# Kernel tuning notes

Measured on AMD Instinct MI355X. Metric: run time of the kernel, lower is better.

The kernel has to match this reference:

```python
import jax, jax.numpy as jnp
import numpy as np

N = 4096
IN_C = 256
F = 256          # num_filter
C = 40           # label_dim
KP1 = 3          # K+1 Chebyshev orders (K=2 hardcoded in forward)
E = 131072
TWO_PI = 2.0 * np.pi


def build_Lc(edges, q, edge_weight, n):
    """Conjugate of the normalized magnetic Laplacian (max_eigen=2 => L = -A_n * exp(i*Theta)).
    We return conj(L) because the original code swaps L.real/L.imag when feeding `process`,
    which is algebraically O_i = i * conj(T_i(L))."""
    row, col = edges[0], edges[1]
    A = jnp.zeros((n, n), jnp.float32).at[row, col].add(edge_weight)  # duplicates sum, as in coo_matrix
    A_sym = 0.5 * (A + A.T)
    d = A_sym.sum(axis=0)
    d = jnp.where(d == 0, 1.0, d)
    dinv = d ** -0.5
    A_n = dinv[:, None] * A_sym * dinv[None, :]
    Theta = TWO_PI * q * (A - A.T)
    # conj(L) = -A_n * exp(-i*Theta)
    return (-A_n).astype(jnp.complex64) * jnp.exp(-1j * Theta.astype(jnp.complex64))


def cheb_layer(Lc, Xr, Xi, W, b):
    """One ChebConv_Qin_Direct layer. Output = sum_i (i * T_i(conj(L)) @ Xc) @ W_i + bias,
    which reproduces the real/imag-swapped `process` of the original module."""
    Xc = (Xr + 1j * Xi).astype(jnp.complex64)      # [N, d]
    Z0 = Xc
    Z1 = Lc @ Xc                                   # sparse-equivalent spmm, dense here
    Z2 = 2.0 * (Lc @ Z1) - Z0                      # Chebyshev recursion T2 = 2 L T1 - T0
    Yc = 1j * (Z0 @ W[0].astype(jnp.complex64)
               + Z1 @ W[1].astype(jnp.complex64)
               + Z2 @ W[2].astype(jnp.complex64))  # [N, out]
    return Yc.real + b, Yc.imag + b


def setup_inputs() -> dict:
    key = jax.random.key(0)
    k = jax.random.split(key, 8)
    stdv1 = 1.0 / np.sqrt(F)
    return {
        "real": jax.random.normal(k[0], (N, IN_C), jnp.float32),
        "imag": jax.random.normal(k[1], (N, IN_C), jnp.float32),
        "edges": jax.random.randint(k[2], (2, E), 0, N),
        "q": jnp.float32(0.25),
        "edge_weight": jax.random.uniform(k[3], (E,), jnp.float32),
        "W1": jax.random.uniform(k[4], (KP1, IN_C, F), jnp.float32, -stdv1, stdv1),
        "b1": jnp.zeros((1, F), jnp.float32),
        "W2": jax.random.uniform(k[5], (KP1, F, F), jnp.float32, -stdv1, stdv1),
        "b2": jnp.zeros((1, F), jnp.float32),
        "Wc": jax.random.normal(k[6], (C, 2 * F), jnp.float32) * (1.0 / np.sqrt(2 * F)),
        "bc": jnp.zeros((C,), jnp.float32),
    }


def reference(real, imag, edges, q, edge_weight, W1, b1, W2, b2, Wc, bc):
    n = real.shape[0]
    Lc = build_Lc(edges, q, edge_weight, n)        # same L is rebuilt each layer in the original
    r, i = cheb_layer(Lc, real, imag, W1, b1)
    r, i = cheb_layer(Lc, r, i, W2, b2)            # activation=False, dropout=False
    x = jnp.concatenate([r, i], axis=-1)           # [N, 2F]
    logits = x @ Wc.T + bc                         # Conv1d(kernel_size=1) == linear
    return jax.nn.log_softmax(logits, axis=-1)     # [N, C]
```

## Files before the change

kernel.cpp:

```cpp
#include <hip/hip_runtime.h>
#include <cmath>

#define N_NODES 4096
#define FDIM    256
#define CDIM    40
#define NEDGE   131072
#define CAP     256
#define HBITS   20
#define HSIZE   (1 << HBITS)
#define TWO_PI_F 6.28318530717958647692f

typedef __bf16 bf16;
typedef __bf16 bf16x2 __attribute__((ext_vector_type(2)));
typedef __bf16 bf16x4 __attribute__((ext_vector_type(4)));
typedef __bf16 bf16x8 __attribute__((ext_vector_type(8)));
typedef float  f32x4  __attribute__((ext_vector_type(4)));

static constexpr size_t NF = (size_t)N_NODES * FDIM;

struct __align__(16) Entry { float lr, li; int col, pad; };

__device__ __forceinline__ void gld_lds16(const bf16* g, bf16* s) {
    __builtin_amdgcn_global_load_lds(
        (const __attribute__((address_space(1))) void*)g,
        (__attribute__((address_space(3))) void*)s,
        16, 0, 0);
}

__device__ __forceinline__ unsigned cell_hash(unsigned cell) {
    return (cell * 2654435761u) >> (32 - HBITS);
}

__global__ void hash_insert(const int* __restrict__ edges,
                            const float* __restrict__ ew,
                            int* __restrict__ hkey, float* __restrict__ hval,
                            float* __restrict__ rowsum, float* __restrict__ colsum) {
    int e = blockIdx.x * blockDim.x + threadIdx.x;
    if (e >= NEDGE) return;
    int r = edges[e], c = edges[NEDGE + e];
    float wv = ew[e];
    atomicAdd(rowsum + r, wv);
    atomicAdd(colsum + c, wv);
    unsigned cell = (unsigned)r * N_NODES + c;
    unsigned h = cell_hash(cell);
    for (;;) {
        int old = atomicCAS(hkey + h, 0, (int)(cell + 1));
        if (old == 0 || old == (int)(cell + 1)) { atomicAdd(hval + h, wv); break; }
        h = (h + 1) & (HSIZE - 1);
    }
}

__global__ __launch_bounds__(256) void hash_to_ell(
    const int* __restrict__ hkey, const float* __restrict__ hval,
    const float* __restrict__ rowsum, const float* __restrict__ colsum,
    const float* __restrict__ qptr,
    int* __restrict__ cnt, Entry* __restrict__ ent) {
    int h = blockIdx.x * 256 + threadIdx.x;
    int k = hkey[h];
    if (k == 0) return;
    unsigned cell = (unsigned)(k - 1);
    int i = cell >> 12, j = cell & 4095;
    float a = hval[h];
    float b = 0.f;
    bool mirror = false;
    if (i == j) { b = a; mirror = true; }
    else {
        unsigned mcell = (unsigned)j * N_NODES + i;
        unsigned hh = cell_hash(mcell);
        for (;;) {
            int kk = hkey[hh];
            if (kk == (int)(mcell + 1)) { b = hval[hh]; mirror = true; break; }
            if (kk == 0) break;
            hh = (hh + 1) & (HSIZE - 1);
        }
    }
    float di = 0.5f * (rowsum[i] + colsum[i]); if (di == 0.f) di = 1.f;
    float dj = 0.5f * (rowsum[j] + colsum[j]); if (dj == 0.f) dj = 1.f;
    float an = 0.5f * (a + b) / sqrtf(di * dj);
    float s, c;
    sincosf(TWO_PI_F * qptr[0] * (a - b), &s, &c);
    int pos = atomicAdd(cnt + i, 1);
    if (pos < CAP) {
        Entry en; en.lr = -an * c; en.li = an * s; en.col = j; en.pad = 0;
        ent[(size_t)i * CAP + pos] = en;
    }
    if (!mirror) {
        int pos2 = atomicAdd(cnt + j, 1);
        if (pos2 < CAP) {
            Entry en; en.lr = -an * c; en.li = -an * s; en.col = i; en.pad = 0;
            ent[(size_t)j * CAP + pos2] = en;
        }
    }
}

__global__ __launch_bounds__(256) void cast_in2(const float* __restrict__ Xr,
                                                const float* __restrict__ Xi,
                                                bf16* __restrict__ Xr16,
                                                bf16* __restrict__ Xi16,
                                                bf16* __restrict__ XC) {
    int idx = blockIdx.x * 256 + threadIdx.x;
    float vr = Xr[idx], vi = Xi[idx];
    Xr16[idx] = (bf16)vr; Xi16[idx] = (bf16)vi;
    bf16x2 p; p[0] = (bf16)vr; p[1] = (bf16)vi;
    ((bf16x2*)XC)[idx] = p;
}

#define NWT (256 * 768)
__global__ __launch_bounds__(256) void cast_weights(
    const float* __restrict__ W1, const float* __restrict__ W2,
    const float* __restrict__ Wc,
    bf16* __restrict__ W1t, bf16* __restrict__ W2t, bf16* __restrict__ Wcb) {
    int idx = blockIdx.x * 256 + threadIdx.x;
    if (idx < 2 * NWT) {
        const float* W = (idx < NWT) ? W1 : W2;
        bf16* Wt = (idx < NWT) ? W1t : W2t;
        int id = (idx < NWT) ? idx : idx - NWT;
        int nout = id / 768, kk = id - nout * 768;
        int o = kk >> 8, k = kk & 255;
        Wt[id] = (bf16)W[((size_t)o * 256 + k) * 256 + nout];
    } else {
        int id = idx - 2 * NWT;
        if (id < 48 * 512) {
            int row = id >> 9, k = id & 511;
            Wcb[id] = (row < CDIM) ? (bf16)Wc[row * 512 + k] : (bf16)0.f;
        }
    }
}

__global__ __launch_bounds__(256) void spmm_k(
    const int* __restrict__ cnt, const Entry* __restrict__ ent,
    const bf16* __restrict__ XC,
    const bf16* __restrict__ C0C,
    float alpha, float beta,
    bf16* __restrict__ Zr, bf16* __restrict__ Zi, bf16* __restrict__ ZC)
{
    __shared__ f32x4 redR[3][64];
    __shared__ f32x4 redI[3][64];

    const int wave = threadIdx.x >> 6, lane = threadIdx.x & 63;
    const int row = blockIdx.x;
    int n1 = cnt[row]; if (n1 > CAP) n1 = CAP;
    const Entry* erow = ent + (size_t)row * CAP;

    float ar[4] = {}, ai[4] = {};
    int e = wave;
    for (; e + 12 < n1; e += 16) {
        Entry e0 = erow[e];
        Entry e1 = erow[e + 4];
        Entry e2 = erow[e + 8];
        Entry e3 = erow[e + 12];
        bf16x8 x0 = *(const bf16x8*)&XC[(size_t)(e0.col & 4095) * 512 + lane * 8];
        bf16x8 x1 = *(const bf16x8*)&XC[(size_t)(e1.col & 4095) * 512 + lane * 8];
        bf16x8 x2 = *(const bf16x8*)&XC[(size_t)(e2.col & 4095) * 512 + lane * 8];
        bf16x8 x3 = *(const bf16x8*)&XC[(size_t)(e3.col & 4095) * 512 + lane * 8];
        #pragma unroll
        for (int c = 0; c < 4; ++c) {
            float xr, xi;
            xr = (float)x0[2 * c]; xi = (float)x0[2 * c + 1];
            ar[c] += e0.lr * xr - e0.li * xi;  ai[c] += e0.lr * xi + e0.li * xr;
            xr = (float)x1[2 * c]; xi = (float)x1[2 * c + 1];
            ar[c] += e1.lr * xr - e1.li * xi;  ai[c] += e1.lr * xi + e1.li * xr;
            xr = (float)x2[2 * c]; xi = (float)x2[2 * c + 1];
            ar[c] += e2.lr * xr - e2.li * xi;  ai[c] += e2.lr * xi + e2.li * xr;
            xr = (float)x3[2 * c]; xi = (float)x3[2 * c + 1];
            ar[c] += e3.lr * xr - e3.li * xi;  ai[c] += e3.lr * xi + e3.li * xr;
        }
    }
    for (; e < n1; e += 4) {
        Entry e0 = erow[e];
        bf16x8 x0 = *(const bf16x8*)&XC[(size_t)(e0.col & 4095) * 512 + lane * 8];
        #pragma unroll
        for (int c = 0; c < 4; ++c) {
            float xr0 = (float)x0[2 * c], xi0 = (float)x0[2 * c + 1];
            ar[c] += e0.lr * xr0 - e0.li * xi0;
            ai[c] += e0.lr * xi0 + e0.li * xr0;
        }
    }

    if (wave != 0) {
        f32x4 r, i;
        #pragma unroll
        for (int c = 0; c < 4; ++c) { r[c] = ar[c]; i[c] = ai[c]; }
        redR[wave - 1][lane] = r;
        redI[wave - 1][lane] = i;
    }
    __syncthreads();
    if (wave != 0) return;

    #pragma unroll
    for (int w = 0; w < 3; ++w) {
        f32x4 r = redR[w][lane], i = redI[w][lane];
        #pragma unroll
        for (int c = 0; c < 4; ++c) { ar[c] += r[c]; ai[c] += i[c]; }
    }

    float vr[4], vi[4];
    if (beta != 0.f) {
        bf16x8 c0 = *(const bf16x8*)&C0C[(size_t)row * 512 + lane * 8];
        #pragma unroll
        for (int c = 0; c < 4; ++c) {
            vr[c] = alpha * ar[c] + beta * (float)c0[2 * c];
            vi[c] = alpha * ai[c] + beta * (float)c0[2 * c + 1];
        }
    } else {
        #pragma unroll
        for (int c = 0; c < 4; ++c) { vr[c] = alpha * ar[c]; vi[c] = alpha * ai[c]; }
    }
    size_t base = (size_t)row * FDIM + lane * 4;
    bf16x4 pr, pi;
    #pragma unroll
    for (int c = 0; c < 4; ++c) { pr[c] = (bf16)vr[c]; pi[c] = (bf16)vi[c]; }
    *(bf16x4*)&Zr[base] = pr;
    *(bf16x4*)&Zi[base] = pi;
    if (ZC) {
        bf16x8 o;
        #pragma unroll
        for (int c = 0; c < 4; ++c) { o[2 * c] = pr[c]; o[2 * c + 1] = pi[c]; }
        *(bf16x8*)&ZC[(size_t)row * 512 + lane * 8] = o;
    }
}

__global__ __launch_bounds__(256) void wapply_mfma(
    const bf16* __restrict__ Z0r, const bf16* __restrict__ Z0i,
    const bf16* __restrict__ Z1r, const bf16* __restrict__ Z1i,
    const bf16* __restrict__ Z2r, const bf16* __restrict__ Z2i,
    const bf16* __restrict__ Wt,
    const float* __restrict__ bias,
    float* __restrict__ O32r, float* __restrict__ O32i,
    bf16* __restrict__ O16r_r, bf16* __restrict__ O16r_i,
    bf16* __restrict__ OC)
{
    __shared__ __align__(16) bf16 sZr[64 * 32];
    __shared__ __align__(16) bf16 sZi[64 * 32];
    __shared__ __align__(16) bf16 sW [64 * 32];

    const int tid  = threadIdx.x;
    const int wave = tid >> 6;
    const int lane = tid & 63;
    const int rowBase = blockIdx.y * 64;
    const int colBase = blockIdx.x * 64;

    const int srow = lane >> 2;
    const int skc  = (lane & 3) * 8;

    f32x4 accSr[2][2] = {}, accSi[2][2] = {};
    const int wm = wave & 1, wn = wave >> 1;
    const int fr = lane & 15;
    const int fk = (lane >> 4) * 8;

    for (int kb = 0; kb < 3 * FDIM; kb += 32) {
        int order = kb >> 8;
        int kloc  = kb & 255;
        if (wave == 0 || wave == 1) {
            const bf16* z;
            if (wave == 0) z = (order == 0) ? Z0r : (order == 1) ? Z1r : Z2r;
            else           z = (order == 0) ? Z0i : (order == 1) ? Z1i : Z2i;
            bf16* s = (wave == 0) ? sZr : sZi;
            const bf16* g = z + (size_t)(rowBase + srow) * FDIM + kloc + skc;
            #pragma unroll
            for (int t = 0; t < 4; ++t)
                gld_lds16(g + (size_t)t * 16 * FDIM, s + t * 512);
        } else if (wave == 2) {
            const bf16* g = Wt + (size_t)(colBase + srow) * 768 + kb + skc;
            #pragma unroll
            for (int t = 0; t < 4; ++t)
                gld_lds16(g + (size_t)t * 16 * 768, sW + t * 512);
        }
        __syncthreads();

        bf16x8 zr[2], zi[2], wv[2];
        #pragma unroll
        for (int m = 0; m < 2; ++m) {
            int r = wm * 32 + m * 16 + fr;
            zr[m] = *(const bf16x8*)&sZr[r * 32 + fk];
            zi[m] = *(const bf16x8*)&sZi[r * 32 + fk];
        }
        #pragma unroll
        for (int n = 0; n < 2; ++n) {
            int c = wn * 32 + n * 16 + fr;
            wv[n] = *(const bf16x8*)&sW[c * 32 + fk];
        }
        #pragma unroll
        for (int m = 0; m < 2; ++m)
            #pragma unroll
            for (int n = 0; n < 2; ++n) {
                accSr[m][n] = __builtin_amdgcn_mfma_f32_16x16x32_bf16(zr[m], wv[n], accSr[m][n], 0, 0, 0);
                accSi[m][n] = __builtin_amdgcn_mfma_f32_16x16x32_bf16(zi[m], wv[n], accSi[m][n], 0, 0, 0);
            }
        __syncthreads();
    }

    #pragma unroll
    for (int m = 0; m < 2; ++m)
        #pragma unroll
        for (int n = 0; n < 2; ++n) {
            int row0 = rowBase + wm * 32 + m * 16 + (lane >> 4) * 4;
            int col  = colBase + wn * 32 + n * 16 + (lane & 15);
            float bv = bias[col];
            #pragma unroll
            for (int r = 0; r < 4; ++r) {
                float vr = bv - accSi[m][n][r];
                float vi = bv + accSr[m][n][r];
                int row = row0 + r;
                size_t idx = (size_t)row * FDIM + col;
                if (O32r) {
                    O32r[idx] = vr; O32i[idx] = vi;
                }
                if (O16r_r) {
                    O16r_r[idx] = (bf16)vr; O16r_i[idx] = (bf16)vi;
                }
                if (OC) {
                    bf16x2 p; p[0] = (bf16)vr; p[1] = (bf16)vi;
                    ((bf16x2*)OC)[idx] = p;
                }
            }
        }
}

__global__ __launch_bounds__(256) void head_mfma(
    const bf16* __restrict__ Yrb,
    const bf16* __restrict__ Yib,
    const bf16* __restrict__ Wcb,
    const float* __restrict__ bc,
    float* __restrict__ out)
{
    __shared__ __align__(16) bf16 sY[64][72];
    __shared__ __align__(16) bf16 sW[48][72];
    __shared__ float sS[64][52];

    const int tid  = threadIdx.x;
    const int wave = tid >> 6;
    const int lane = tid & 63;
    const int r0 = blockIdx.x * 64;

    f32x4 acc[3] = {};

    for (int kb = 0; kb < 512; kb += 64) {
        const bf16* src = (kb < 256) ? Yrb : Yib;
        const int koff = kb & 255;
        #pragma unroll
        for (int e = 0; e < 2; ++e) {
            int idx = tid + e * 256;
            int rr = idx >> 3, kk = (idx & 7) * 8;
            *(bf16x8*)&sY[rr][kk] =
                *(const bf16x8*)&src[(size_t)(r0 + rr) * FDIM + koff + kk];
        }
        #pragma unroll
        for (int e = 0; e < 2; ++e) {
            int idx = tid + e * 256;
            if (idx < 384) {
                int rr = idx >> 3, kk = (idx & 7) * 8;
                *(bf16x8*)&sW[rr][kk] =
                    *(const bf16x8*)&Wcb[(size_t)rr * 512 + kb + kk];
            }
        }
        __syncthreads();
        #pragma unroll
        for (int ks = 0; ks < 2; ++ks) {
            bf16x8 a = *(const bf16x8*)&sY[wave * 16 + (lane & 15)][ks * 32 + (lane >> 4) * 8];
            #pragma unroll
            for (int n = 0; n < 3; ++n) {
                bf16x8 b = *(const bf16x8*)&sW[n * 16 + (lane & 15)][ks * 32 + (lane >> 4) * 8];
                acc[n] = __builtin_amdgcn_mfma_f32_16x16x32_bf16(a, b, acc[n], 0, 0, 0);
            }
        }
        __syncthreads();
    }

    #pragma unroll
    for (int n = 0; n < 3; ++n) {
        int col = n * 16 + (lane & 15);
        int rloc = wave * 16 + (lane >> 4) * 4;
        #pragma unroll
        for (int r = 0; r < 4; ++r)
            sS[rloc + r][col] = acc[n][r];
    }
    __syncthreads();

    if (tid < 64) {
        float mx = -INFINITY;
        #pragma unroll 8
        for (int c = 0; c < CDIM; ++c) {
            float lv = sS[tid][c] + bc[c];
            sS[tid][c] = lv;
            mx = fmaxf(mx, lv);
        }
        float se = 0.f;
        #pragma unroll 8
        for (int c = 0; c < CDIM; ++c) se += expf(sS[tid][c] - mx);
        float lse = mx + logf(se);
        #pragma unroll 8
        for (int c = 0; c < CDIM; ++c)
            out[(size_t)(r0 + tid) * CDIM + c] = sS[tid][c] - lse;
    }
}

extern "C" void kernel_launch(void* const* d_in, const int* in_sizes, int n_in,
                              void* d_out, int out_size, void* d_ws, size_t ws_size,
                              hipStream_t stream) {
    const float* real = (const float*)d_in[0];
    const float* imag = (const float*)d_in[1];
    const int*   edges = (const int*)d_in[2];
    const float* q    = (const float*)d_in[3];
    const float* ew   = (const float*)d_in[4];
    const float* W1   = (const float*)d_in[5];
    const float* b1   = (const float*)d_in[6];
    const float* W2   = (const float*)d_in[7];
    const float* b2   = (const float*)d_in[8];
    const float* Wc   = (const float*)d_in[9];
    const float* bc   = (const float*)d_in[10];
    float* out = (float*)d_out;

    char* w = (char*)d_ws;
    int*      hkey   = (int*)w;   w += (size_t)HSIZE * 4;
    float*    hval   = (float*)w; w += (size_t)HSIZE * 4;
    int*      cnt    = (int*)w;   w += N_NODES * 4;
    float*    rowsum = (float*)w; w += N_NODES * 4;
    float*    colsum = (float*)w; w += N_NODES * 4;
    size_t zero_bytes = (size_t)((char*)w - (char*)d_ws);
    Entry* ent  = (Entry*)w; w += (size_t)N_NODES * CAP * 16;
    bf16* Xr16 = (bf16*)w; w += NF * 2;
    bf16* Xi16 = (bf16*)w; w += NF * 2;
    bf16* XC   = (bf16*)w; w += NF * 4;
    bf16* Z1r  = (bf16*)w; w += NF * 2;
    bf16* Z1i  = (bf16*)w; w += NF * 2;
    bf16* Z1C  = (bf16*)w; w += NF * 4;
    bf16* Z2r  = (bf16*)w; w += NF * 2;
    bf16* Z2i  = (bf16*)w; w += NF * 2;
    float* Y1r32 = (float*)w; w += NF * 4;
    float* Y1i32 = (float*)w; w += NF * 4;
    bf16* Y1rb = (bf16*)w; w += NF * 2;
    bf16* Y1ib = (bf16*)w; w += NF * 2;
    bf16* Y1C  = (bf16*)w; w += NF * 4;
    bf16* Y2rb = (bf16*)w; w += NF * 2;
    bf16* Y2ib = (bf16*)w; w += NF * 2;
    bf16* W1t  = (bf16*)w; w += 256 * 768 * 2;
    bf16* W2t  = (bf16*)w; w += 256 * 768 * 2;
    bf16* Wcb  = (bf16*)w; w += 48 * 512 * 2;

    hipMemsetAsync(d_ws, 0, zero_bytes, stream);

    hash_insert<<<(NEDGE + 255) / 256, 256, 0, stream>>>(edges, ew, hkey, hval,
                                                         rowsum, colsum);
    hash_to_ell<<<HSIZE / 256, 256, 0, stream>>>(hkey, hval, rowsum, colsum,
                                                 q, cnt, ent);

    cast_in2<<<NF / 256, 256, 0, stream>>>(real, imag, Xr16, Xi16, XC);
    cast_weights<<<(2 * NWT + 48 * 512 + 255) / 256, 256, 0, stream>>>(
        W1, W2, Wc, W1t, W2t, Wcb);

    dim3 gW(FDIM / 64, N_NODES / 64);

    spmm_k<<<N_NODES, 256, 0, stream>>>(cnt, ent, XC, nullptr,
                                        1.f, 0.f, Z1r, Z1i, Z1C);
    spmm_k<<<N_NODES, 256, 0, stream>>>(cnt, ent, Z1C, XC,
                                        2.f, -1.f, Z2r, Z2i, nullptr);
    wapply_mfma<<<gW, 256, 0, stream>>>(Xr16, Xi16, Z1r, Z1i, Z2r, Z2i,
                                        W1t, b1,
                                        Y1r32, Y1i32,
                                        Y1rb, Y1ib,
                                        Y1C);

    spmm_k<<<N_NODES, 256, 0, stream>>>(cnt, ent, Y1C, nullptr,
                                        1.f, 0.f, Z1r, Z1i, Z1C);
    spmm_k<<<N_NODES, 256, 0, stream>>>(cnt, ent, Z1C, Y1C,
                                        2.f, -1.f, Z2r, Z2i, nullptr);
    wapply_mfma<<<gW, 256, 0, stream>>>(Y1rb, Y1ib, Z1r, Z1i, Z2r, Z2i,
                                        W2t, b2,
                                        nullptr, nullptr,
                                        Y2rb, Y2ib,
                                        nullptr);

    head_mfma<<<64, 256, 0, stream>>>(Y2rb, Y2ib, Wcb, bc, out);
}
```

Before: 272.7 us.

## Fuse all stages into one cooperative persistent kernel with grid syncs

After: 883.2 us. 3.24x slower.

```diff
diff --git a/kernel.cpp b/kernel.cpp
--- a/kernel.cpp
+++ b/kernel.cpp
@@ -1,5 +1,8 @@
 #include <hip/hip_runtime.h>
+#include <hip/hip_cooperative_groups.h>
 #include <cmath>
+
+namespace cg = cooperative_groups;
 
 #define N_NODES 4096
 #define FDIM    256
@@ -9,6 +12,8 @@
 #define HBITS   20
 #define HSIZE   (1 << HBITS)
 #define TWO_PI_F 6.28318530717958647692f
+#define GRID    512
+#define NWT     (256 * 768)
 
 typedef __bf16 bf16;
 typedef __bf16 bf16x2 __attribute__((ext_vector_type(2)));
@@ -17,8 +22,23 @@
 typedef float  f32x4  __attribute__((ext_vector_type(4)));
 
 static constexpr size_t NF = (size_t)N_NODES * FDIM;
+static constexpr int ZWORDS = 2 * HSIZE + 3 * N_NODES;
 
 struct __align__(16) Entry { float lr, li; int col, pad; };
+
+struct Params {
+    const int* edges; const float* ew; const float* q;
+    const float* real; const float* imag;
+    const float* W1; const float* b1; const float* W2; const float* b2;
+    const float* Wc; const float* bc;
+    int* hkey; float* hval; int* cnt; float* rowsum; float* colsum;
+    Entry* ent;
+    bf16 *Xr16, *Xi16, *XC;
+    bf16 *Z1r, *Z1i, *Z1C, *Z2r, *Z2i;
+    bf16 *Y1rb, *Y1ib, *Y1C, *Y2rb, *Y2ib;
+    bf16 *W1t, *W2t, *Wcb;
+    float* out;
+};
 
 __device__ __forceinline__ void gld_lds16(const bf16* g, bf16* s) {
     __builtin_amdgcn_global_load_lds(
@@ -31,214 +51,198 @@
     return (cell * 2654435761u) >> (32 - HBITS);
 }
 
-__global__ void hash_insert(const int* __restrict__ edges,
-                            const float* __restrict__ ew,
-                            int* __restrict__ hkey, float* __restrict__ hval,
-                            float* __restrict__ rowsum, float* __restrict__ colsum) {
-    int e = blockIdx.x * blockDim.x + threadIdx.x;
-    if (e >= NEDGE) return;
-    int r = edges[e], c = edges[NEDGE + e];
-    float wv = ew[e];
-    atomicAdd(rowsum + r, wv);
-    atomicAdd(colsum + c, wv);
-    unsigned cell = (unsigned)r * N_NODES + c;
-    unsigned h = cell_hash(cell);
-    for (;;) {
-        int old = atomicCAS(hkey + h, 0, (int)(cell + 1));
-        if (old == 0 || old == (int)(cell + 1)) { atomicAdd(hval + h, wv); break; }
-        h = (h + 1) & (HSIZE - 1);
-    }
-}
-
-__global__ __launch_bounds__(256) void hash_to_ell(
-    const int* __restrict__ hkey, const float* __restrict__ hval,
-    const float* __restrict__ rowsum, const float* __restrict__ colsum,
-    const float* __restrict__ qptr,
-    int* __restrict__ cnt, Entry* __restrict__ ent) {
-    int h = blockIdx.x * 256 + threadIdx.x;
-    int k = hkey[h];
-    if (k == 0) return;
-    unsigned cell = (unsigned)(k - 1);
-    int i = cell >> 12, j = cell & 4095;
-    float a = hval[h];
-    float b = 0.f;
-    bool mirror = false;
-    if (i == j) { b = a; mirror = true; }
-    else {
-        unsigned mcell = (unsigned)j * N_NODES + i;
-        unsigned hh = cell_hash(mcell);
+__device__ void init_stage(const Params& p, int gtid, int stride) {
+    int* zw = (int*)p.hkey;
+    for (int w0 = gtid; w0 < ZWORDS; w0 += stride) zw[w0] = 0;
+
+    for (int idx = gtid; idx < (int)NF; idx += stride) {
+        float vr = p.real[idx], vi = p.imag[idx];
+        p.Xr16[idx] = (bf16)vr; p.Xi16[idx] = (bf16)vi;
+        bf16x2 pp; pp[0] = (bf16)vr; pp[1] = (bf16)vi;
+        ((bf16x2*)p.XC)[idx] = pp;
+    }
+    for (int idx = gtid; idx < 2 * NWT + 48 * 512; idx += stride) {
+        if (idx < 2 * NWT) {
+            const float* W = (idx < NWT) ? p.W1 : p.W2;
+            bf16* Wt = (idx < NWT) ? p.W1t : p.W2t;
+            int id = (idx < NWT) ? idx : idx - NWT;
+            int nout = id / 768, kk = id - nout * 768;
+            int o = kk >> 8, k = kk & 255;
+            Wt[id] = (bf16)W[((size_t)o * 256 + k) * 256 + nout];
+        } else {
+            int id = idx - 2 * NWT;
+            int row = id >> 9, k = id & 511;
+            p.Wcb[id] = (row < CDIM) ? (bf16)p.Wc[row * 512 + k] : (bf16)0.f;
+        }
+    }
+}
+
+__device__ void hash_stage(const Params& p, int gtid, int stride) {
+    for (int e = gtid; e < NEDGE; e += stride) {
+        int r = p.edges[e], c = p.edges[NEDGE + e];
+        float wv = p.ew[e];
+        atomicAdd(p.rowsum + r, wv);
+        atomicAdd(p.colsum + c, wv);
+        unsigned cell = (unsigned)r * N_NODES + c;
+        unsigned h = cell_hash(cell);
         for (;;) {
-            int kk = hkey[hh];
-            if (kk == (int)(mcell + 1)) { b = hval[hh]; mirror = true; break; }
-            if (kk == 0) break;
-            hh = (hh + 1) & (HSIZE - 1);
-        }
-    }
-    float di = 0.5f * (rowsum[i] + colsum[i]); if (di == 0.f) di = 1.f;
-    float dj = 0.5f * (rowsum[j] + colsum[j]); if (dj == 0.f) dj = 1.f;
-    float an = 0.5f * (a + b) / sqrtf(di * dj);
-    float s, c;
-    sincosf(TWO_PI_F * qptr[0] * (a - b), &s, &c);
-    int pos = atomicAdd(cnt + i, 1);
-    if (pos < CAP) {
-        Entry en; en.lr = -an * c; en.li = an * s; en.col = j; en.pad = 0;
-        ent[(size_t)i * CAP + pos] = en;
-    }
-    if (!mirror) {
-        int pos2 = atomicAdd(cnt + j, 1);
-        if (pos2 < CAP) {
-            Entry en; en.lr = -an * c; en.li = -an * s; en.col = i; en.pad = 0;
-            ent[(size_t)j * CAP + pos2] = en;
-        }
-    }
-}
-
-__global__ __launch_bounds__(256) void cast_in2(const float* __restrict__ Xr,
-                                                const float* __restrict__ Xi,
-                                                bf16* __restrict__ Xr16,
-                                                bf16* __restrict__ Xi16,
-                                                bf16* __restrict__ XC) {
-    int idx = blockIdx.x * 256 + threadIdx.x;
-    float vr = Xr[idx], vi = Xi[idx];
-    Xr16[idx] = (bf16)vr; Xi16[idx] = (bf16)vi;
-    bf16x2 p; p[0] = (bf16)vr; p[1] = (bf16)vi;
-    ((bf16x2*)XC)[idx] = p;
-}
-
-#define NWT (256 * 768)
-__global__ __launch_bounds__(256) void cast_weights(
-    const float* __restrict__ W1, const float* __restrict__ W2,
-    const float* __restrict__ Wc,
-    bf16* __restrict__ W1t, bf16* __restrict__ W2t, bf16* __restrict__ Wcb) {
-    int idx = blockIdx.x * 256 + threadIdx.x;
-    if (idx < 2 * NWT) {
-        const float* W = (idx < NWT) ? W1 : W2;
-        bf16* Wt = (idx < NWT) ? W1t : W2t;
-        int id = (idx < NWT) ? idx : idx - NWT;
-        int nout = id / 768, kk = id - nout * 768;
-        int o = kk >> 8, k = kk & 255;
-        Wt[id] = (bf16)W[((size_t)o * 256 + k) * 256 + nout];
-    } else {
-        int id = idx - 2 * NWT;
-        if (id < 48 * 512) {
-            int row = id >> 9, k = id & 511;
-            Wcb[id] = (row < CDIM) ? (bf16)Wc[row * 512 + k] : (bf16)0.f;
-        }
-    }
-}
-
-__global__ __launch_bounds__(256) void spmm_k(
-    const int* __restrict__ cnt, const Entry* __restrict__ ent,
-    const bf16* __restrict__ XC,
-    const bf16* __restrict__ C0C,
-    float alpha, float beta,
-    bf16* __restrict__ Zr, bf16* __restrict__ Zi, bf16* __restrict__ ZC)
+            int old = atomicCAS(p.hkey + h, 0, (int)(cell + 1));
+            if (old == 0 || old == (int)(cell + 1)) { atomicAdd(p.hval + h, wv); break; }
+            h = (h + 1) & (HSIZE - 1);
+        }
+    }
+}
+
+__device__ void ell_stage(const Params& p, int gtid, int stride) {
+    for (int h = gtid; h < HSIZE; h += stride) {
+        int k = p.hkey[h];
+        if (k == 0) continue;
+        unsigned cell = (unsigned)(k - 1);
+        int i = cell >> 12, j = cell & 4095;
+        float a = p.hval[h];
+        float b = 0.f;
+        bool mirror = false;
+        if (i == j) { b = a; mirror = true; }
+        else {
+            unsigned mcell = (unsigned)j * N_NODES + i;
+            unsigned hh = cell_hash(mcell);
+            for (;;) {
+                int kk = p.hkey[hh];
+                if (kk == (int)(mcell + 1)) { b = p.hval[hh]; mirror = true; break; }
+                if (kk == 0) break;
+                hh = (hh + 1) & (HSIZE - 1);
+            }
+        }
+        float di = 0.5f * (p.rowsum[i] + p.colsum[i]); if (di == 0.f) di = 1.f;
+        float dj = 0.5f * (p.rowsum[j] + p.colsum[j]); if (dj == 0.f) dj = 1.f;
+        float an = 0.5f * (a + b) / sqrtf(di * dj);
+        float s, c;
+        sincosf(TWO_PI_F * p.q[0] * (a - b), &s, &c);
+        int pos = atomicAdd(p.cnt + i, 1);
+        if (pos < CAP) {
+            Entry en; en.lr = -an * c; en.li = an * s; en.col = j; en.pad = 0;
+            p.ent[(size_t)i * CAP + pos] = en;
+        }
+        if (!mirror) {
+            int pos2 = atomicAdd(p.cnt + j, 1);
+            if (pos2 < CAP) {
+                Entry en; en.lr = -an * c; en.li = -an * s; en.col = i; en.pad = 0;
+                p.ent[(size_t)j * CAP + pos2] = en;
+            }
+        }
+    }
+}
+
+__device__ void spmm_stage(const int* __restrict__ cnt, const Entry* __restrict__ ent,
+                           const bf16* __restrict__ XC, const bf16* __restrict__ C0C,
+                           float alpha, float beta,
+                           bf16* __restrict__ Zr, bf16* __restrict__ Zi,
+                           bf16* __restrict__ ZC, char* smem, int bid)
 {
-    __shared__ f32x4 redR[3][64];
-    __shared__ f32x4 redI[3][64];
-
+    f32x4* redR = (f32x4*)smem;
+    f32x4* redI = redR + 192;
     const int wave = threadIdx.x >> 6, lane = threadIdx.x & 63;
-    const int row = blockIdx.x;
-    int n1 = cnt[row]; if (n1 > CAP) n1 = CAP;
-    const Entry* erow = ent + (size_t)row * CAP;
-
-    float ar[4] = {}, ai[4] = {};
-    int e = wave;
-    for (; e + 12 < n1; e += 16) {
-        Entry e0 = erow[e];
-        Entry e1 = erow[e + 4];
-        Entry e2 = erow[e + 8];
-        Entry e3 = erow[e + 12];
-        bf16x8 x0 = *(const bf16x8*)&XC[(size_t)(e0.col & 4095) * 512 + lane * 8];
-        bf16x8 x1 = *(const bf16x8*)&XC[(size_t)(e1.col & 4095) * 512 + lane * 8];
-        bf16x8 x2 = *(const bf16x8*)&XC[(size_t)(e2.col & 4095) * 512 + lane * 8];
-        bf16x8 x3 = *(const bf16x8*)&XC[(size_t)(e3.col & 4095) * 512 + lane * 8];
-        #pragma unroll
-        for (int c = 0; c < 4; ++c) {
-            float xr, xi;
-            xr = (float)x0[2 * c]; xi = (float)x0[2 * c + 1];
-            ar[c] += e0.lr * xr - e0.li * xi;  ai[c] += e0.lr * xi + e0.li * xr;
-            xr = (float)x1[2 * c]; xi = (float)x1[2 * c + 1];
-            ar[c] += e1.lr * xr - e1.li * xi;  ai[c] += e1.lr * xi + e1.li * xr;
-            xr = (float)x2[2 * c]; xi = (float)x2[2 * c + 1];
-            ar[c] += e2.lr * xr - e2.li * xi;  ai[c] += e2.lr * xi + e2.li * xr;
-            xr = (float)x3[2 * c]; xi = (float)x3[2 * c + 1];
-            ar[c] += e3.lr * xr - e3.li * xi;  ai[c] += e3.lr * xi + e3.li * xr;
-        }
-    }
-    for (; e < n1; e += 4) {
-        Entry e0 = erow[e];
-        bf16x8 x0 = *(const bf16x8*)&XC[(size_t)(e0.col & 4095) * 512 + lane * 8];
-        #pragma unroll
-        for (int c = 0; c < 4; ++c) {
-            float xr0 = (float)x0[2 * c], xi0 = (float)x0[2 * c + 1];
-            ar[c] += e0.lr * xr0 - e0.li * xi0;
-            ai[c] += e0.lr * xi0 + e0.li * xr0;
-        }
-    }
-
-    if (wave != 0) {
-        f32x4 r, i;
-        #pragma unroll
-        for (int c = 0; c < 4; ++c) { r[c] = ar[c]; i[c] = ai[c]; }
-        redR[wave - 1][lane] = r;
-        redI[wave - 1][lane] = i;
-    }
-    __syncthreads();
-    if (wave != 0) return;
-
-    #pragma unroll
-    for (int w = 0; w < 3; ++w) {
-        f32x4 r = redR[w][lane], i = redI[w][lane];
-        #pragma unroll
-        for (int c = 0; c < 4; ++c) { ar[c] += r[c]; ai[c] += i[c]; }
-    }
-
-    float vr[4], vi[4];
-    if (beta != 0.f) {
-        bf16x8 c0 = *(const bf16x8*)&C0C[(size_t)row * 512 + lane * 8];
-        #pragma unroll
-        for (int c = 0; c < 4; ++c) {
-            vr[c] = alpha * ar[c] + beta * (float)c0[2 * c];
-            vi[c] = alpha * ai[c] + beta * (float)c0[2 * c + 1];
-        }
-    } else {
-        #pragma unroll
-        for (int c = 0; c < 4; ++c) { vr[c] = alpha * ar[c]; vi[c] = alpha * ai[c]; }
-    }
-    size_t base = (size_t)row * FDIM + lane * 4;
-    bf16x4 pr, pi;
-    #pragma unroll
-    for (int c = 0; c < 4; ++c) { pr[c] = (bf16)vr[c]; pi[c] = (bf16)vi[c]; }
-    *(bf16x4*)&Zr[base] = pr;
-    *(bf16x4*)&Zi[base] = pi;
-    if (ZC) {
-        bf16x8 o;
-        #pragma unroll
-        for (int c = 0; c < 4; ++c) { o[2 * c] = pr[c]; o[2 * c + 1] = pi[c]; }
-        *(bf16x8*)&ZC[(size_t)row * 512 + lane * 8] = o;
-    }
-}
-
-__global__ __launch_bounds__(256) void wapply_mfma(
-    const bf16* __restrict__ Z0r, const bf16* __restrict__ Z0i,
-    const bf16* __restrict__ Z1r, const bf16* __restrict__ Z1i,
-    const bf16* __restrict__ Z2r, const bf16* __restrict__ Z2i,
-    const bf16* __restrict__ Wt,
-    const float* __restrict__ bias,
-    float* __restrict__ O32r, float* __restrict__ O32i,
-    bf16* __restrict__ O16r_r, bf16* __restrict__ O16r_i,
-    bf16* __restrict__ OC)
+
+    for (int rr = 0; rr < 8; ++rr) {
+        const int row = bid * 8 + rr;
+        int n1 = cnt[row]; if (n1 > CAP) n1 = CAP;
+        const Entry* erow = ent + (size_t)row * CAP;
+
+        float ar[4] = {}, ai[4] = {};
+        int e = wave;
+        for (; e + 12 < n1; e += 16) {
+            Entry e0 = erow[e];
+            Entry e1 = erow[e + 4];
+            Entry e2 = erow[e + 8];
+            Entry e3 = erow[e + 12];
+            bf16x8 x0 = *(const bf16x8*)&XC[(size_t)(e0.col & 4095) * 512 + lane * 8];
+            bf16x8 x1 = *(const bf16x8*)&XC[(size_t)(e1.col & 4095) * 512 + lane * 8];
+            bf16x8 x2 = *(const bf16x8*)&XC[(size_t)(e2.col & 4095) * 512 + lane * 8];
+            bf16x8 x3 = *(const bf16x8*)&XC[(size_t)(e3.col & 4095) * 512 + lane * 8];
+            #pragma unroll
+            for (int c = 0; c < 4; ++c) {
+                float xr, xi;
+                xr = (float)x0[2 * c]; xi = (float)x0[2 * c + 1];
+                ar[c] += e0.lr * xr - e0.li * xi;  ai[c] += e0.lr * xi + e0.li * xr;
+                xr = (float)x1[2 * c]; xi = (float)x1[2 * c + 1];
+                ar[c] += e1.lr * xr - e1.li * xi;  ai[c] += e1.lr * xi + e1.li * xr;
+                xr = (float)x2[2 * c]; xi = (float)x2[2 * c + 1];
+                ar[c] += e2.lr * xr - e2.li * xi;  ai[c] += e2.lr * xi + e2.li * xr;
+                xr = (float)x3[2 * c]; xi = (float)x3[2 * c + 1];
+                ar[c] += e3.lr * xr - e3.li * xi;  ai[c] += e3.lr * xi + e3.li * xr;
+            }
+        }
+        for (; e < n1; e += 4) {
+            Entry e0 = erow[e];
+            bf16x8 x0 = *(const bf16x8*)&XC[(size_t)(e0.col & 4095) * 512 + lane * 8];
+            #pragma unroll
+            for (int c = 0; c < 4; ++c) {
+                float xr0 = (float)x0[2 * c], xi0 = (float)x0[2 * c + 1];
+                ar[c] += e0.lr * xr0 - e0.li * xi0;
+                ai[c] += e0.lr * xi0 + e0.li * xr0;
+            }
+        }
+
+        if (wave != 0) {
+            f32x4 r, i;
+            #pragma unroll
+            for (int c = 0; c < 4; ++c) { r[c] = ar[c]; i[c] = ai[c]; }
+            redR[(wave - 1) * 64 + lane] = r;
+            redI[(wave - 1) * 64 + lane] = i;
+        }
+        __syncthreads();
+        if (wave == 0) {
+            #pragma unroll
+            for (int w = 0; w < 3; ++w) {
+                f32x4 r = redR[w * 64 + lane], i = redI[w * 64 + lane];
+                #pragma unroll
+                for (int c = 0; c < 4; ++c) { ar[c] += r[c]; ai[c] += i[c]; }
+            }
+            float vr[4], vi[4];
+            if (beta != 0.f) {
+                bf16x8 c0 = *(const bf16x8*)&C0C[(size_t)row * 512 + lane * 8];
+                #pragma unroll
+                for (int c = 0; c < 4; ++c) {
+                    vr[c] = alpha * ar[c] + beta * (float)c0[2 * c];
+                    vi[c] = alpha * ai[c] + beta * (float)c0[2 * c + 1];
+                }
+            } else {
+                #pragma unroll
+                for (int c = 0; c < 4; ++c) { vr[c] = alpha * ar[c]; vi[c] = alpha * ai[c]; }
+            }
+            size_t base = (size_t)row * FDIM + lane * 4;
+            bf16x4 pr, pi;
+            #pragma unroll
+            for (int c = 0; c < 4; ++c) { pr[c] = (bf16)vr[c]; pi[c] = (bf16)vi[c]; }
+            *(bf16x4*)&Zr[base] = pr;
+            *(bf16x4*)&Zi[base] = pi;
+            if (ZC) {
+                bf16x8 o;
+                #pragma unroll
+                for (int c = 0; c < 4; ++c) { o[2 * c] = pr[c]; o[2 * c + 1] = pi[c]; }
+                *(bf16x8*)&ZC[(size_t)row * 512 + lane * 8] = o;
+            }
+        }
+        __syncthreads();
+    }
+}
+
+__device__ void wapply_stage(const bf16* __restrict__ Z0r, const bf16* __restrict__ Z0i,
+                             const bf16* __restrict__ Z1r, const bf16* __restrict__ Z1i,
+                             const bf16* __restrict__ Z2r, const bf16* __restrict__ Z2i,
+                             const bf16* __restrict__ Wt, const float* __restrict__ bias,
+                             bf16* __restrict__ Or, bf16* __restrict__ Oi,
+                             bf16* __restrict__ OC, char* smem, int bid)
 {
-    __shared__ __align__(16) bf16 sZr[64 * 32];
-    __shared__ __align__(16) bf16 sZi[64 * 32];
-    __shared__ __align__(16) bf16 sW [64 * 32];
+    bf16* sZr = (bf16*)smem;
+    bf16* sZi = (bf16*)(smem + 4096);
+    bf16* sW  = (bf16*)(smem + 8192);
 
     const int tid  = threadIdx.x;
     const int wave = tid >> 6;
     const int lane = tid & 63;
-    const int rowBase = blockIdx.y * 64;
-    const int colBase = blockIdx.x * 64;
+    const int rowBase = (bid >> 2) * 64;
+    const int colBase = (bid & 3) * 64;
 
     const int srow = lane >> 2;
     const int skc  = (lane & 3) * 8;
@@ -301,37 +305,28 @@
             for (int r = 0; r < 4; ++r) {
                 float vr = bv - accSi[m][n][r];
                 float vi = bv + accSr[m][n][r];
-                int row = row0 + r;
-                size_t idx = (size_t)row * FDIM + col;
-                if (O32r) {
-                    O32r[idx] = vr; O32i[idx] = vi;
+                size_t idx = (size_t)(row0 + r) * FDIM + col;
+                Or[idx] = (bf16)vr; Oi[idx] = (bf16)vi;
+                if (OC) {
+                    bf16x2 pp; pp[0] = (bf16)vr; pp[1] = (bf16)vi;
+                    ((bf16x2*)OC)[idx] = pp;
                 }
-                if (O16r_r) {
-                    O16r_r[idx] = (bf16)vr; O16r_i[idx] = (bf16)vi;
-                }
-                if (OC) {
-                    bf16x2 p; p[0] = (bf16)vr; p[1] = (bf16)vi;
-                    ((bf16x2*)OC)[idx] = p;
-                }
-            }
-        }
-}
-
-__global__ __launch_bounds__(256) void head_mfma(
-    const bf16* __restrict__ Yrb,
-    const bf16* __restrict__ Yib,
-    const bf16* __restrict__ Wcb,
-    const float* __restrict__ bc,
-    float* __restrict__ out)
+            }
+        }
+}
+
+__device__ void head_stage(const bf16* __restrict__ Yrb, const bf16* __restrict__ Yib,
+                           const bf16* __restrict__ Wcb, const float* __restrict__ bc,
+                           float* __restrict__ out, char* smem, int bid)
 {
-    __shared__ __align__(16) bf16 sY[64][72];
-    __shared__ __align__(16) bf16 sW[48][72];
-    __shared__ float sS[64][52];
+    bf16*  sY = (bf16*)smem;
+    bf16*  sW = (bf16*)(smem + 9216);
+    float* sS = (float*)(smem + 9216 + 6912);
 
     const int tid  = threadIdx.x;
     const int wave = tid >> 6;
     const int lane = tid & 63;
-    const int r0 = blockIdx.x * 64;
+    const int r0 = bid * 64;
 
     f32x4 acc[3] = {};
 
@@ -342,7 +337,7 @@
         for (int e = 0; e < 2; ++e) {
             int idx = tid + e * 256;
             int rr = idx >> 3, kk = (idx & 7) * 8;
-            *(bf16x8*)&sY[rr][kk] =
+            *(bf16x8*)&sY[rr * 72 + kk] =
                 *(const bf16x8*)&src[(size_t)(r0 + rr) * FDIM + koff + kk];
         }
         #pragma unroll
@@ -350,17 +345,17 @@
             int idx = tid + e * 256;
             if (idx < 384) {
                 int rr = idx >> 3, kk = (idx & 7) * 8;
-                *(bf16x8*)&sW[rr][kk] =
+                *(bf16x8*)&sW[rr * 72 + kk] =
                     *(const bf16x8*)&Wcb[(size_t)rr * 512 + kb + kk];
             }
         }
         __syncthreads();
         #pragma unroll
         for (int ks = 0; ks < 2; ++ks) {
-            bf16x8 a = *(const bf16x8*)&sY[wave * 16 + (lane & 15)][ks * 32 + (lane >> 4) * 8];
+            bf16x8 a = *(const bf16x8*)&sY[(wave * 16 + (lane & 15)) * 72 + ks * 32 + (lane >> 4) * 8];
             #pragma unroll
             for (int n = 0; n < 3; ++n) {
-                bf16x8 b = *(const bf16x8*)&sW[n * 16 + (lane & 15)][ks * 32 + (lane >> 4) * 8];
+                bf16x8 b = *(const bf16x8*)&sW[(n * 16 + (lane & 15)) * 72 + ks * 32 + (lane >> 4) * 8];
                 acc[n] = __builtin_amdgcn_mfma_f32_16x16x32_bf16(a, b, acc[n], 0, 0, 0);
             }
         }
@@ -373,7 +368,7 @@
         int rloc = wave * 16 + (lane >> 4) * 4;
         #pragma unroll
         for (int r = 0; r < 4; ++r)
-            sS[rloc + r][col] = acc[n][r];
+            sS[(rloc + r) * 52 + col] = acc[n][r];
     }
     __syncthreads();
 
@@ -381,95 +376,152 @@
         float mx = -INFINITY;
         #pragma unroll 8
         for (int c = 0; c < CDIM; ++c) {
-            float lv = sS[tid][c] + bc[c];
-            sS[tid][c] = lv;
+            float lv = sS[tid * 52 + c] + bc[c];
+            sS[tid * 52 + c] = lv;
             mx = fmaxf(mx, lv);
         }
         float se = 0.f;
         #pragma unroll 8
-        for (int c = 0; c < CDIM; ++c) se += expf(sS[tid][c] - mx);
+        for (int c = 0; c < CDIM; ++c) se += expf(sS[tid * 52 + c] - mx);
         float lse = mx + logf(se);
         #pragma unroll 8
         for (int c = 0; c < CDIM; ++c)
-            out[(size_t)(r0 + tid) * CDIM + c] = sS[tid][c] - lse;
-    }
+            out[(size_t)(r0 + tid) * CDIM + c] = sS[tid * 52 + c] - lse;
+    }
+    __syncthreads();
+}
+
+__global__ __launch_bounds__(256, 2) void mega(Params p) {
+    cg::grid_group grid = cg::this_grid();
+    __shared__ __align__(16) char smem[29440];
+
+    const int bid  = blockIdx.x;
+    const int tid  = threadIdx.x;
+    const int gtid = bid * 256 + tid;
+    const int stride = gridDim.x * 256;
+
+    init_stage(p, gtid, stride);
+    grid.sync();
+    hash_stage(p, gtid, stride);
+    grid.sync();
+    ell_stage(p, gtid, stride);
+    grid.sync();
+
+    spmm_stage(p.cnt, p.ent, p.XC, nullptr, 1.f, 0.f, p.Z1r, p.Z1i, p.Z1C, smem, bid);
+    grid.sync();
+    spmm_stage(p.cnt, p.ent, p.Z1C, p.XC, 2.f, -1.f, p.Z2r, p.Z2i, nullptr, smem, bid);
+    grid.sync();
+    if (bid < 256)
+        wapply_stage(p.Xr16, p.Xi16, p.Z1r, p.Z1i, p.Z2r, p.Z2i,
+                     p.W1t, p.b1, p.Y1rb, p.Y1ib, p.Y1C, smem, bid);
+    grid.sync();
+
+    spmm_stage(p.cnt, p.ent, p.Y1C, nullptr, 1.f, 0.f, p.Z1r, p.Z1i, p.Z1C, smem, bid);
+    grid.sync();
+    spmm_stage(p.cnt, p.ent, p.Z1C, p.Y1C, 2.f, -1.f, p.Z2r, p.Z2i, nullptr, smem, bid);
+    grid.sync();
+    if (bid < 256)
+        wapply_stage(p.Y1rb, p.Y1ib, p.Z1r, p.Z1i, p.Z2r, p.Z2i,
+                     p.W2t, p.b2, p.Y2rb, p.Y2ib, nullptr, smem, bid);
+    grid.sync();
+
+    if (bid < 64)
+        head_stage(p.Y2rb, p.Y2ib, p.Wcb, p.bc, p.out, smem, bid);
+}
+
+__global__ __launch_bounds__(256) void k_init(Params p) {
+    init_stage(p, blockIdx.x * 256 + threadIdx.x, gridDim.x * 256);
+}
+__global__ __launch_bounds__(256) void k_hash(Params p) {
+    hash_stage(p, blockIdx.x * 256 + threadIdx.x, gridDim.x * 256);
+}
+__global__ __launch_bounds__(256) void k_ell(Params p) {
+    ell_stage(p, blockIdx.x * 256 + threadIdx.x, gridDim.x * 256);
+}
+__global__ __launch_bounds__(256) void k_spmm(const int* cnt, const Entry* ent,
+                                              const bf16* XC, const bf16* C0C,
+                                              float alpha, float beta,
+                                              bf16* Zr, bf16* Zi, bf16* ZC) {
+    __shared__ __align__(16) char smem[6144];
+    spmm_stage(cnt, ent, XC, C0C, alpha, beta, Zr, Zi, ZC, smem, blockIdx.x);
+}
+__global__ __launch_bounds__(256) void k_wapply(const bf16* Z0r, const bf16* Z0i,
+                                                const bf16* Z1r, const bf16* Z1i,
+                                                const bf16* Z2r, const bf16* Z2i,
+                                                const bf16* Wt, const float* bias,
+                                                bf16* Or, bf16* Oi, bf16* OC) {
+    __shared__ __align__(16) char smem[12288];
+    wapply_stage(Z0r, Z0i, Z1r, Z1i, Z2r, Z2i, Wt, bias, Or, Oi, OC, smem, blockIdx.x);
+}
+__global__ __launch_bounds__(256) void k_head(const bf16* Yrb, const bf16* Yib,
+                                              const bf16* Wcb, const float* bc,
+                                              float* out) {
+    __shared__ __align__(16) char smem[29440];
+    head_stage(Yrb, Yib, Wcb, bc, out, smem, blockIdx.x);
 }
 
 extern "C" void kernel_launch(void* const* d_in, const int* in_sizes, int n_in,
                               void* d_out, int out_size, void* d_ws, size_t ws_size,
                               hipStream_t stream) {
-    const float* real = (const float*)d_in[0];
-    const float* imag = (const float*)d_in[1];
-    const int*   edges = (const int*)d_in[2];
-    const float* q    = (const float*)d_in[3];
-    const float* ew   = (const float*)d_in[4];
-    const float* W1   = (const float*)d_in[5];
-    const float* b1   = (const float*)d_in[6];
-    const float* W2   = (const float*)d_in[7];
-    const float* b2   = (const float*)d_in[8];
-    const float* Wc   = (const float*)d_in[9];
-    const float* bc   = (const float*)d_in[10];
-    float* out = (float*)d_out;
+    Params p;
+    p.real = (const float*)d_in[0];
+    p.imag = (const float*)d_in[1];
+    p.edges = (const int*)d_in[2];
+    p.q    = (const float*)d_in[3];
+    p.ew   = (const float*)d_in[4];
+    p.W1   = (const float*)d_in[5];
+    p.b1   = (const float*)d_in[6];
+    p.W2   = (const float*)d_in[7];
+    p.b2   = (const float*)d_in[8];
+    p.Wc   = (const float*)d_in[9];
+    p.bc   = (const float*)d_in[10];
+    p.out  = (float*)d_out;
 
     char* w = (char*)d_ws;
-    int*      hkey   = (int*)w;   w += (size_t)HSIZE * 4;
-    float*    hval   = (float*)w; w += (size_t)HSIZE * 4;
-    int*      cnt    = (int*)w;   w += N_NODES * 4;
-    float*    rowsum = (float*)w; w += N_NODES * 4;
-    float*    colsum = (float*)w; w += N_NODES * 4;
-    size_t zero_bytes = (size_t)((char*)w - (char*)d_ws);
-    Entry* ent  = (Entry*)w; w += (size_t)N_NODES * CAP * 16;
-    bf16* Xr16 = (bf16*)w; w += NF * 2;
-    bf16* Xi16 = (bf16*)w; w += NF * 2;
-    bf16* XC   = (bf16*)w; w += NF * 4;
-    bf16* Z1r  = (bf16*)w; w += NF * 2;
-    bf16* Z1i  = (bf16*)w; w += NF * 2;
-    bf16* Z1C  = (bf16*)w; w += NF * 4;
-    bf16* Z2r  = (bf16*)w; w += NF * 2;
-    bf16* Z2i  = (bf16*)w; w += NF * 2;
-    float* Y1r32 = (float*)w; w += NF * 4;
-    float* Y1i32 = (float*)w; w += NF * 4;
-    bf16* Y1rb = (bf16*)w; w += NF * 2;
-    bf16* Y1ib = (bf16*)w; w += NF * 2;
-    bf16* Y1C  = (bf16*)w; w += NF * 4;
-    bf16* Y2rb = (bf16*)w; w += NF * 2;
-    bf16* Y2ib = (bf16*)w; w += NF * 2;
-    bf16* W1t  = (bf16*)w; w += 256 * 768 * 2;
-    bf16* W2t  = (bf16*)w; w += 256 * 768 * 2;
-    bf16* Wcb  = (bf16*)w; w += 48 * 512 * 2;
-
-    hipMemsetAsync(d_ws, 0, zero_bytes, stream);
-
-    hash_insert<<<(NEDGE + 255) / 256, 256, 0, stream>>>(edges, ew, hkey, hval,
-                                                         rowsum, colsum);
-    hash_to_ell<<<HSIZE / 256, 256, 0, stream>>>(hkey, hval, rowsum, colsum,
-                                                 q, cnt, ent);
-
-    cast_in2<<<NF / 256, 256, 0, stream>>>(real, imag, Xr16, Xi16, XC);
-    cast_weights<<<(2 * NWT + 48 * 512 + 255) / 256, 256, 0, stream>>>(
-        W1, W2, Wc, W1t, W2t, Wcb);
-
-    dim3 gW(FDIM / 64, N_NODES / 64);
-
-    spmm_k<<<N_NODES, 256, 0, stream>>>(cnt, ent, XC, nullptr,
-                                        1.f, 0.f, Z1r, Z1i, Z1C);
-    spmm_k<<<N_NODES, 256, 0, stream>>>(cnt, ent, Z1C, XC,
-                                        2.f, -1.f, Z2r, Z2i, nullptr);
-    wapply_mfma<<<gW, 256, 0, stream>>>(Xr16, Xi16, Z1r, Z1i, Z2r, Z2i,
-                                        W1t, b1,
-                                        Y1r32, Y1i32,
-                                        Y1rb, Y1ib,
-                                        Y1C);
-
-    spmm_k<<<N_NODES, 256, 0, stream>>>(cnt, ent, Y1C, nullptr,
-                                        1.f, 0.f, Z1r, Z1i, Z1C);
-    spmm_k<<<N_NODES, 256, 0, stream>>>(cnt, ent, Z1C, Y1C,
-                                        2.f, -1.f, Z2r, Z2i, nullptr);
-    wapply_mfma<<<gW, 256, 0, stream>>>(Y1rb, Y1ib, Z1r, Z1i, Z2r, Z2i,
-                                        W2t, b2,
-                                        nullptr, nullptr,
-                                        Y2rb, Y2ib,
-                                        nullptr);
-
-    head_mfma<<<64, 256, 0, stream>>>(Y2rb, Y2ib, Wcb, bc, out);
-}
+    p.hkey   = (int*)w;   w += (size_t)HSIZE * 4;
+    p.hval   = (float*)w; w += (size_t)HSIZE * 4;
+    p.cnt    = (int*)w;   w += N_NODES * 4;
+    p.rowsum = (float*)w; w += N_NODES * 4;
+    p.colsum = (float*)w; w += N_NODES * 4;
+    p.ent    = (Entry*)w; w += (size_t)N_NODES * CAP * 16;
+    p.Xr16 = (bf16*)w; w += NF * 2;
+    p.Xi16 = (bf16*)w; w += NF * 2;
+    p.XC   = (bf16*)w; w += NF * 4;
+    p.Z1r  = (bf16*)w; w += NF * 2;
+    p.Z1i  = (bf16*)w; w += NF * 2;
+    p.Z1C  = (bf16*)w; w += NF * 4;
+    p.Z2r  = (bf16*)w; w += NF * 2;
+    p.Z2i  = (bf16*)w; w += NF * 2;
+    p.Y1rb = (bf16*)w; w += NF * 2;
+    p.Y1ib = (bf16*)w; w += NF * 2;
+    p.Y1C  = (bf16*)w; w += NF * 4;
+    p.Y2rb = (bf16*)w; w += NF * 2;
+    p.Y2ib = (bf16*)w; w += NF * 2;
+    p.W1t  = (bf16*)w; w += 256 * 768 * 2;
+    p.W2t  = (bf16*)w; w += 256 * 768 * 2;
+    p.Wcb  = (bf16*)w; w += 48 * 512 * 2;
+
+    void* args[] = { &p };
+    hipError_t err = hipLaunchCooperativeKernel((void*)mega, dim3(GRID), dim3(256),
+                                                args, 0, stream);
+    if (err != hipSuccess) {
+        (void)hipGetLastError();
+        dim3 b(256);
+        k_init<<<GRID, b, 0, stream>>>(p);
+        k_hash<<<GRID, b, 0, stream>>>(p);
+        k_ell<<<GRID, b, 0, stream>>>(p);
+        k_spmm<<<GRID, b, 0, stream>>>(p.cnt, p.ent, p.XC, nullptr,
+                                       1.f, 0.f, p.Z1r, p.Z1i, p.Z1C);
+        k_spmm<<<GRID, b, 0, stream>>>(p.cnt, p.ent, p.Z1C, p.XC,
+                                       2.f, -1.f, p.Z2r, p.Z2i, nullptr);
+        k_wapply<<<256, b, 0, stream>>>(p.Xr16, p.Xi16, p.Z1r, p.Z1i, p.Z2r, p.Z2i,
+                                        p.W1t, p.b1, p.Y1rb, p.Y1ib, p.Y1C);
+        k_spmm<<<GRID, b, 0, stream>>>(p.cnt, p.ent, p.Y1C, nullptr,
+                                       1.f, 0.f, p.Z1r, p.Z1i, p.Z1C);
+        k_spmm<<<GRID, b, 0, stream>>>(p.cnt, p.ent, p.Z1C, p.Y1C,
+                                       2.f, -1.f, p.Z2r, p.Z2i, nullptr);
+        k_wapply<<<256, b, 0, stream>>>(p.Y1rb, p.Y1ib, p.Z1r, p.Z1i, p.Z2r, p.Z2i,
+                                        p.W2t, p.b2, p.Y2rb, p.Y2ib, nullptr);
+        k_head<<<64, b, 0, stream>>>(p.Y2rb, p.Y2ib, p.Wcb, p.bc, p.out);
+    }
+}
```
